# Optimization experiments

Measured on AMD Instinct MI355X. Metric: run time of the kernel, lower is better.

The kernel has to match this reference:

```python
import jax, jax.numpy as jnp
import numpy as np

T, N, E = 64, 10000, 160000
NIN, NHID, NOUT = 64, 128, 64

def _xavier(key, shape):
    # xavier_normal_ for Linear/GCNConv lin weights of shape [out, in]
    std = jnp.sqrt(2.0 / (shape[0] + shape[1])).astype(jnp.float32)
    return std * jax.random.normal(key, shape, dtype=jnp.float32)

def setup_inputs() -> dict:
    key = jax.random.key(0)
    ks = jax.random.split(key, 12)
    x = jax.random.normal(ks[0], (T, N, NIN), dtype=jnp.float32)
    src = jax.random.randint(ks[1], (E,), 0, N)
    dst = jax.random.randint(ks[2], (E,), 0, N)
    edge_index = jnp.stack([src, dst])  # [2, E], PyG convention src->dst
    m_in = dst   # receiver index per edge (one-hot row of incidence matrix)
    m_out = src  # sender index per edge
    b = 0.1 * jnp.ones((NHID,), jnp.float32)
    return {
        "x": x, "edge_index": edge_index, "m_in": m_in, "m_out": m_out,
        "Wi": _xavier(ks[3], (NHID, NIN + NHID)), "bi": b,
        "Wf": _xavier(ks[4], (NHID, NIN + NHID)), "bf": b,
        "Wo": _xavier(ks[5], (NHID, NIN + NHID)), "bo": b,
        "Wg": _xavier(ks[6], (NHID, NIN + NHID)), "bg": b,
        "W1": _xavier(ks[7], (NHID, 2 * NHID)), "b1": b,
        "Wc": _xavier(ks[8], (NOUT, NHID)), "bc": 0.1 * jnp.ones((NOUT,), jnp.float32),
    }

def reference(x, edge_index, m_in, m_out, Wi, bi, Wf, bf, Wo, bo, Wg, bg, W1, b1, Wc, bc):
    n = x.shape[1]
    src, dst = edge_index[0], edge_index[1]
    loop = jnp.arange(n)
    s = jnp.concatenate([src, loop])  # self-loops appended (GCNConv default)
    d = jnp.concatenate([dst, loop])
    deg = jax.ops.segment_sum(jnp.ones_like(d, x.dtype), d, num_segments=n)
    dinv = jnp.where(deg > 0, deg, 1.0) ** -0.5  # deg>=1 with self-loops
    norm = (dinv[s] * dinv[d])[:, None]

    def gcn(z, W, b):
        zw = z @ W.T                    # [n, out]
        return jax.ops.segment_sum(zw[s] * norm, d, num_segments=n) + b

    def step(carry, xt):
        h, c = carry
        comb = jnp.concatenate([xt, h], axis=-1)  # [n, n_in+n_hid]
        i = jax.nn.sigmoid(gcn(comb, Wi, bi))
        f = jax.nn.sigmoid(gcn(comb, Wf, bf))
        o = jax.nn.sigmoid(gcn(comb, Wo, bo))
        g = jnp.tanh(gcn(comb, Wg, bg))
        c = f * c + i * g
        h = o * jnp.tanh(c)
        return (h, c), None

    h0 = jnp.zeros((n, NHID), x.dtype)
    (h, _), _ = jax.lax.scan(step, (h0, h0), x)

    # node2edge: concat receiver and sender hidden states  [E, 2*n_hid]
    e = jnp.concatenate([h[m_in], h[m_out]], axis=-1)
    e = jax.nn.relu(e @ W1.T + b1)  # dropout p=0.0 -> identity
    # edge2node: scatter-sum edge features to receiver nodes
    nodes = jax.ops.segment_sum(e, m_in, num_segments=n)
    return gcn(nodes, Wc, bc)
```

## Files before the change

### kernel.cpp

```cpp
#include <hip/hip_runtime.h>
#include <math.h>

#define NIN 64
#define NHID 128
#define NOUT 64

typedef __bf16 bf16x8 __attribute__((ext_vector_type(8)));
typedef float  floatx4 __attribute__((ext_vector_type(4)));

__device__ __forceinline__ float sigmoidf(float x){ return 1.0f/(1.0f+expf(-x)); }
__device__ __forceinline__ float b2f_lo(unsigned p){ unsigned b = p<<16; return __uint_as_float(b); }
__device__ __forceinline__ float b2f_hi(unsigned p){ unsigned b = p & 0xffff0000u; return __uint_as_float(b); }
__device__ __forceinline__ unsigned f2pk(float lo, float hi){
  __bf16 a=(__bf16)lo, b=(__bf16)hi;
  unsigned short ua, ub;
  __builtin_memcpy(&ua,&a,2); __builtin_memcpy(&ub,&b,2);
  return (unsigned)ua | ((unsigned)ub<<16);
}

__global__ void k_deg_init(int* __restrict__ deg, int n){
  int v = blockIdx.x*256 + threadIdx.x;
  if(v<n) deg[v] = 1;
}
__global__ void k_deg_count(const int* __restrict__ dst, int E, int* __restrict__ deg){
  int e = blockIdx.x*256 + threadIdx.x;
  if(e<E) atomicAdd(&deg[dst[e]], 1);
}
__global__ void k_dinv(const int* __restrict__ deg, float* __restrict__ dinv, int n){
  int v = blockIdx.x*256 + threadIdx.x;
  if(v<n) dinv[v] = rsqrtf((float)deg[v]);
}
__global__ __launch_bounds__(1024) void k_scan(const int* __restrict__ deg,
    int* __restrict__ row_ptr, int* __restrict__ fill, int n){
  __shared__ int lds[1024];
  __shared__ int s_carry;
  if(threadIdx.x==0) s_carry=0;
  __syncthreads();
  int nchunk=(n+1023)/1024;
  for(int ch=0; ch<nchunk; ++ch){
    int v = ch*1024 + threadIdx.x;
    int val = (v<n)? (deg[v]-1) : 0;
    lds[threadIdx.x]=val;
    __syncthreads();
    for(int off=1; off<1024; off<<=1){
      int t=(threadIdx.x>=off)? lds[threadIdx.x-off] : 0;
      __syncthreads();
      lds[threadIdx.x]+=t;
      __syncthreads();
    }
    int incl=lds[threadIdx.x];
    int carry=s_carry;
    if(v<n){ row_ptr[v]=carry+incl-val; fill[v]=carry+incl-val; }
    __syncthreads();
    if(threadIdx.x==1023) s_carry=carry+lds[1023];
    __syncthreads();
  }
  if(threadIdx.x==0) row_ptr[n]=s_carry;
}
__global__ void k_fill(const int* __restrict__ src, const int* __restrict__ dst, int E,
                       int* __restrict__ fill, int* __restrict__ ecol){
  int e = blockIdx.x*256 + threadIdx.x;
  if(e<E){
    int d = dst[e];
    int pos = atomicAdd(&fill[d], 1);
    ecol[pos] = src[e];
  }
}

__global__ void k_prep_wb(const float* __restrict__ Wi, const float* __restrict__ Wf,
                          const float* __restrict__ Wo, const float* __restrict__ Wg,
                          __bf16* __restrict__ Wb){
  int idx = blockIdx.x*256 + threadIdx.x;
  if(idx >= 32*6*64*8) return;
  int jj = idx & 7;
  int L  = (idx >> 3) & 63;
  int t  = idx >> 9;
  int kt = t - (t/6)*6, CT = t/6;
  int colj = CT*16 + (L & 15);
  int k    = kt*32 + ((L >> 4) << 3) + jj;
  int gate = colj >> 7, jg = colj & 127;
  const float* W = (gate==0)? Wi : (gate==1)? Wf : (gate==2)? Wo : Wg;
  Wb[idx] = (__bf16)W[jg*192 + k];
}
__global__ void k_prep_w1(const float* __restrict__ W1, float* __restrict__ W1t){
  int idx = blockIdx.x*256 + threadIdx.x;
  if(idx >= 128*256) return;
  int k = idx >> 8, j = idx & 255;
  W1t[idx] = (j<128)? W1[j*256+k] : W1[(j-128)*256+128+k];
}
__global__ void k_prep_wc(const float* __restrict__ Wc, float* __restrict__ Wct){
  int idx = blockIdx.x*256 + threadIdx.x;
  if(idx >= 128*64) return;
  int k = idx/64, j = idx%64;
  Wct[idx] = Wc[j*128+k];
}

__global__ void k_init(unsigned* __restrict__ hpA, unsigned* __restrict__ hpB,
                       float* __restrict__ cbuf, __bf16* __restrict__ xs,
                       int NP, int T){
  int i = blockIdx.x*256 + threadIdx.x;
  if(i < (NP+1)*64){ hpA[i]=0u; hpB[i]=0u; }
  if(i < NP*128) cbuf[i]=0.f;
  if(i < T*64){ int t=i>>6, f=i&63; xs[((size_t)t*(NP+1) + NP)*64 + f] = (__bf16)0.f; }
}

__global__ void k_xscale(const float* __restrict__ x, const float* __restrict__ dinv,
                         __bf16* __restrict__ xs, int n, int NP){
  int i = blockIdx.x*256 + threadIdx.x;
  if(i >= n*8) return;
  int t = blockIdx.y;
  float dv = dinv[i>>3];
  const float4* xp = (const float4*)(x + (size_t)t*(size_t)n*64) + (size_t)i*2;
  float4 a = xp[0], b = xp[1];
  bf16x8 o;
  o[0]=(__bf16)(a.x*dv); o[1]=(__bf16)(a.y*dv); o[2]=(__bf16)(a.z*dv); o[3]=(__bf16)(a.w*dv);
  o[4]=(__bf16)(b.x*dv); o[5]=(__bf16)(b.y*dv); o[6]=(__bf16)(b.z*dv); o[7]=(__bf16)(b.w*dv);
  *(bf16x8*)(xs + ((size_t)t*(NP+1))*64 + (size_t)i*8) = o;
}

__global__ __launch_bounds__(256,4) void k_step(
    const __bf16* __restrict__ xst,
    const unsigned* __restrict__ hp_prev,
    unsigned* __restrict__ hp_cur,
    float* __restrict__ cbuf,
    float* __restrict__ hbuf,
    const int* __restrict__ row_ptr, const int* __restrict__ ecol,
    const float* __restrict__ dinv, const __bf16* __restrict__ Wb,
    const float* __restrict__ bi, const float* __restrict__ bf_,
    const float* __restrict__ bo, const float* __restrict__ bg,
    int n, int NP, int last)
{
  __shared__ __align__(16) __bf16 s_a[6*544];
  __shared__ int   s_col[1024];
  __shared__ int   s_deg[16];
  __shared__ int   s_beg[16];
  __shared__ float s_dv[16];
  const int tid=threadIdx.x, wv=tid>>6, l=tid&63;
  const int l15=l&15, quad=l>>4;
  const int v0=blockIdx.x*16;

  if(tid<16){
    int v=v0+tid;
    int beg=(v<n)? row_ptr[v]:0, end=(v<n)? row_ptr[v+1]:0;
    s_beg[tid]=beg; s_deg[tid]=end-beg;
    s_dv[tid]=(v<n)? dinv[v]:0.f;
  }
  __syncthreads();
  for(int idx=tid; idx<1024; idx+=256){
    int m=idx>>6, kk=idx&63;
    s_col[idx]=(kk<s_deg[m])? ecol[s_beg[m]+kk] : NP;
  }
  __syncthreads();

  float ax[4], alo[4], ahi[4];
  int K;
  {
    int d0=s_deg[4*wv+0]; d0=d0>64?64:d0;
    int d1=s_deg[4*wv+1]; d1=d1>64?64:d1;
    int d2=s_deg[4*wv+2]; d2=d2>64?64:d2;
    int d3=s_deg[4*wv+3]; d3=d3>64?64:d3;
    int m01=d0>d1?d0:d1, m23=d2>d3?d2:d3;
    K=m01>m23?m01:m23;
  }
  #pragma unroll
  for(int i=0;i<4;++i){
    int v=v0+4*wv+i;
    ax[i]=(float)xst[(size_t)v*64+l];
    unsigned p=hp_prev[(size_t)v*64+l];
    alo[i]=b2f_lo(p); ahi[i]=b2f_hi(p);
  }
  const int* cr=&s_col[(4*wv)*64];
  #pragma unroll 2
  for(int kk=0;kk<K;++kk){
    #pragma unroll
    for(int i=0;i<4;++i){
      int u=cr[i*64+kk];
      float xv=(float)xst[(size_t)u*64+l];
      unsigned p=hp_prev[(size_t)u*64+l];
      ax[i]+=xv; alo[i]+=b2f_lo(p); ahi[i]+=b2f_hi(p);
    }
  }
  #pragma unroll
  for(int i=0;i<4;++i){
    int m=4*wv+i, d=s_deg[m];
    if(d>64){
      for(int e2=s_beg[m]+64;e2<s_beg[m]+d;++e2){
        int u=ecol[e2];
        ax[i]+=(float)xst[(size_t)u*64+l];
        unsigned p=hp_prev[(size_t)u*64+l];
        alo[i]+=b2f_lo(p); ahi[i]+=b2f_hi(p);
      }
    }
  }
  {
    int kt0=l>>5, q0=(l>>3)&3, j0=l&7;
    int L2=2*l, kt1=2+(L2>>5), q1=(L2>>3)&3, j1=L2&7;
    #pragma unroll
    for(int i=0;i<4;++i){
      int m=4*wv+i; float dv=s_dv[m];
      s_a[kt0*544+q0*136+m*8+j0]=(__bf16)(dv*ax[i]);
      *(__shared__ unsigned*)&s_a[kt1*544+q1*136+m*8+j1]=f2pk(dv*alo[i],dv*ahi[i]);
    }
  }
  __syncthreads();

  bf16x8 af[6];
  #pragma unroll
  for(int kt=0;kt<6;++kt)
    af[kt]=*(__shared__ bf16x8*)&s_a[kt*544+quad*136+l15*8];

  #pragma unroll
  for(int h2=0;h2<2;++h2){
    const int ct=2*wv+h2;
    const int jg=16*ct+l15;
    floatx4 acc[4];
    #pragma unroll
    for(int g=0;g<4;++g){
      const float* bsel = (g==0)? bi : (g==1)? bf_ : (g==2)? bo : bg;
      float b=bsel[jg];
      floatx4 a={b,b,b,b};
      const __bf16* bp=Wb + (size_t)((8*g+ct)*6)*512 + (size_t)l*8;
      #pragma unroll
      for(int kt=0;kt<6;++kt)
        a=__builtin_amdgcn_mfma_f32_16x16x32_bf16(af[kt],*(const bf16x8*)(bp+kt*512),a,0,0,0);
      acc[g]=a;
    }
    #pragma unroll
    for(int r=0;r<4;++r){
      int m=quad*4+r, v=v0+m;
      float I=sigmoidf(acc[0][r]);
      float F=sigmoidf(acc[1][r]);
      float O=sigmoidf(acc[2][r]);
      float G=tanhf  (acc[3][r]);
      size_t coff=(size_t)v*128+jg;
      float cn=F*cbuf[coff]+I*G;
      cbuf[coff]=cn;
      float hn=O*tanhf(cn);
      float hs=s_dv[m]*hn;
      float hs2=__shfl_xor(hs,1,64);
      if((l15&1)==0)
        hp_cur[(size_t)v*64+(jg>>1)]=f2pk(hs,hs2);
      if(last) hbuf[coff]=hn;
    }
  }
}

__global__ __launch_bounds__(256) void k_head1(const float* __restrict__ h,
    const float* __restrict__ W1t, float* __restrict__ Hio, int n){
  __shared__ float s_h[16][NHID];
  int v0 = blockIdx.x*16;
  for(int i=threadIdx.x; i<16*NHID; i+=256){
    int m = i/NHID, k = i - m*NHID;
    int v = v0 + m;
    s_h[m][k] = (v<n)? h[(size_t)v*NHID + k] : 0.0f;
  }
  __syncthreads();
  int j = threadIdx.x;
  float acc[16];
  #pragma unroll
  for(int m=0;m<16;++m) acc[m]=0.f;
  for(int k=0;k<NHID;++k){
    float w = W1t[k*256 + j];
    #pragma unroll
    for(int m=0;m<16;++m) acc[m] = fmaf(w, s_h[m][k], acc[m]);
  }
  for(int m=0;m<16;++m){
    int v = v0 + m;
    if(v >= n) break;
    Hio[(size_t)v*256 + j] = acc[m];
  }
}
__global__ __launch_bounds__(256) void k_e2n(const float* __restrict__ Hio,
    const int* __restrict__ row_ptr, const int* __restrict__ col,
    const float* __restrict__ b1, float* __restrict__ nodes, int n){
  int wv = threadIdx.x >> 6, lane = threadIdx.x & 63;
  int v = blockIdx.x*4 + wv;
  if(v >= n) return;
  float base0 = Hio[(size_t)v*256 + lane]      + b1[lane];
  float base1 = Hio[(size_t)v*256 + 64 + lane] + b1[64+lane];
  float a0=0.f, a1=0.f;
  int beg=row_ptr[v], end=row_ptr[v+1];
  int e=beg;
  for(; e+1<end; e+=2){
    int u0 = col[e], u1 = col[e+1];
    float p0 = Hio[(size_t)u0*256 + 128 + lane];
    float q0 = Hio[(size_t)u0*256 + 192 + lane];
    float p1 = Hio[(size_t)u1*256 + 128 + lane];
    float q1 = Hio[(size_t)u1*256 + 192 + lane];
    a0 += fmaxf(base0 + p0, 0.0f) + fmaxf(base0 + p1, 0.0f);
    a1 += fmaxf(base1 + q0, 0.0f) + fmaxf(base1 + q1, 0.0f);
  }
  if(e<end){
    int u = col[e];
    a0 += fmaxf(base0 + Hio[(size_t)u*256 + 128 + lane], 0.0f);
    a1 += fmaxf(base1 + Hio[(size_t)u*256 + 192 + lane], 0.0f);
  }
  nodes[(size_t)v*NHID + lane]      = a0;
  nodes[(size_t)v*NHID + 64 + lane] = a1;
}
__global__ __launch_bounds__(64) void k_head2(const float* __restrict__ nodes,
    const float* __restrict__ Wct, float* __restrict__ tmp, int n){
  __shared__ float s_n[16][NHID];
  int v0 = blockIdx.x*16;
  for(int i=threadIdx.x; i<16*NHID; i+=64){
    int m = i/NHID, k = i - m*NHID;
    int v = v0 + m;
    s_n[m][k] = (v<n)? nodes[(size_t)v*NHID + k] : 0.0f;
  }
  __syncthreads();
  int j = threadIdx.x;
  float acc[16];
  #pragma unroll
  for(int m=0;m<16;++m) acc[m]=0.f;
  for(int k=0;k<NHID;++k){
    float w = Wct[k*64 + j];
    #pragma unroll
    for(int m=0;m<16;++m) acc[m] = fmaf(w, s_n[m][k], acc[m]);
  }
  for(int m=0;m<16;++m){
    int v = v0 + m;
    if(v >= n) break;
    tmp[(size_t)v*64 + j] = acc[m];
  }
}
__global__ __launch_bounds__(256) void k_final(const float* __restrict__ tmp,
    const int* __restrict__ row_ptr, const int* __restrict__ col,
    const float* __restrict__ dinv, const float* __restrict__ bc,
    float* __restrict__ out, int n){
  int wv = threadIdx.x >> 6, lane = threadIdx.x & 63;
  int v = blockIdx.x*4 + wv;
  if(v >= n) return;
  float dv = dinv[v];
  float acc = dv*dv*tmp[(size_t)v*64 + lane];
  int beg=row_ptr[v], end=row_ptr[v+1];
  int e=beg;
  for(; e+1<end; e+=2){
    int u0 = col[e], u1 = col[e+1];
    float d0 = dinv[u0], d1 = dinv[u1];
    float t0 = tmp[(size_t)u0*64 + lane];
    float t1 = tmp[(size_t)u1*64 + lane];
    acc = fmaf(dv*d0, t0, acc);
    acc = fmaf(dv*d1, t1, acc);
  }
  if(e<end){
    int u = col[e];
    acc = fmaf(dv*dinv[u], tmp[(size_t)u*64 + lane], acc);
  }
  out[(size_t)v*64 + lane] = acc + bc[lane];
}

extern "C" void kernel_launch(void* const* d_in, const int* in_sizes, int n_in,
                              void* d_out, int out_size, void* d_ws, size_t ws_size,
                              hipStream_t stream) {
  (void)n_in; (void)ws_size;
  const float* x  = (const float*)d_in[0];
  const int*   ei = (const int*)d_in[1];
  const float* Wi = (const float*)d_in[4];  const float* bi  = (const float*)d_in[5];
  const float* Wf = (const float*)d_in[6];  const float* bf_ = (const float*)d_in[7];
  const float* Wo = (const float*)d_in[8];  const float* bo  = (const float*)d_in[9];
  const float* Wg = (const float*)d_in[10]; const float* bg  = (const float*)d_in[11];
  const float* W1 = (const float*)d_in[12]; const float* b1  = (const float*)d_in[13];
  const float* Wc = (const float*)d_in[14]; const float* bc  = (const float*)d_in[15];
  float* out = (float*)d_out;

  const int E = in_sizes[2];
  const int n = out_size / NOUT;
  const int T = in_sizes[0] / (n * NIN);
  const int ntiles = (n + 15)/16;
  const int NP = ntiles*16;
  const int* srcl = ei;
  const int* dstl = ei + E;

  char* p = (char*)d_ws;
  auto alloc = [&](size_t bytes){ char* r = p; p += ((bytes + 255)/256)*256; return r; };
  int*      deg     = (int*)     alloc((size_t)n*4);
  float*    dinv    = (float*)   alloc((size_t)n*4);
  int*      row_ptr = (int*)     alloc((size_t)(n+1)*4);
  int*      fill    = (int*)     alloc((size_t)n*4);
  int*      ecol    = (int*)     alloc((size_t)E*4);
  __bf16*   Wb      = (__bf16*)  alloc((size_t)32*6*64*8*2);
  float*    W1t     = (float*)   alloc((size_t)128*256*4);
  float*    Wct     = (float*)   alloc((size_t)128*64*4);
  __bf16*   xs      = (__bf16*)  alloc((size_t)T*(NP+1)*64*2);
  unsigned* hpA     = (unsigned*)alloc((size_t)(NP+1)*64*4);
  unsigned* hpB     = (unsigned*)alloc((size_t)(NP+1)*64*4);
  float*    cbuf    = (float*)   alloc((size_t)NP*128*4);
  float*    hbuf    = (float*)   alloc((size_t)NP*128*4);
  float*    Hio     = (float*)   alloc((size_t)NP*256*4);
  float*    nodes   = (float*)   alloc((size_t)n*NHID*4);
  float*    tmp     = (float*)   alloc((size_t)NP*64*4);

  int gn = (n+255)/256;
  int gE = (E+255)/256;

  k_deg_init <<<gn, 256, 0, stream>>>(deg, n);
  k_deg_count<<<gE, 256, 0, stream>>>(dstl, E, deg);
  k_dinv     <<<gn, 256, 0, stream>>>(deg, dinv, n);
  k_scan     <<<1, 1024, 0, stream>>>(deg, row_ptr, fill, n);
  k_fill     <<<gE, 256, 0, stream>>>(srcl, dstl, E, fill, ecol);

  k_prep_wb<<<(32*6*64*8+255)/256, 256, 0, stream>>>(Wi, Wf, Wo, Wg, Wb);
  k_prep_w1<<<(128*256+255)/256, 256, 0, stream>>>(W1, W1t);
  k_prep_wc<<<(128*64+255)/256, 256, 0, stream>>>(Wc, Wct);

  k_init<<<((NP*128)+255)/256, 256, 0, stream>>>(hpA, hpB, cbuf, xs, NP, T);
  k_xscale<<<dim3((n*8+255)/256, T), 256, 0, stream>>>(x, dinv, xs, n, NP);

  for(int t=0; t<T; ++t){
    const __bf16* xst = xs + (size_t)t*(size_t)(NP+1)*64;
    const unsigned* hp = (t & 1)? hpB : hpA;
    unsigned*       hc = (t & 1)? hpA : hpB;
    k_step<<<ntiles, 256, 0, stream>>>(xst, hp, hc, cbuf, hbuf, row_ptr, ecol, dinv,
                                       Wb, bi, bf_, bo, bg, n, NP, (t==T-1)?1:0);
  }

  k_head1<<<ntiles, 256, 0, stream>>>(hbuf, W1t, Hio, n);
  k_e2n  <<<(n+3)/4, 256, 0, stream>>>(Hio, row_ptr, ecol, b1, nodes, n);
  k_head2<<<(n+15)/16, 64, 0, stream>>>(nodes, Wct, tmp, n);
  k_final<<<(n+3)/4, 256, 0, stream>>>(tmp, row_ptr, ecol, dinv, bc, out, n);
}
```

Baseline: 1.789 ms.

## Precompute x-part neighbor aggregation for all timesteps outside the recurrent loop

The GCN aggregation of the input features x does not depend on the hidden state, so it is moved out of the 64 sequential step kernels into one batched k_xgather kernel. That kernel writes pre-normalized bf16 A-tiles in MFMA layout for every timestep. The step kernel now gathers only neighbor hidden states and loads the x tiles directly into registers. It also runs with 512 threads, one output column tile per wave, which spreads the gate computation across more waves per block. The cost is extra memory for the precomputed tiles and an fp32 gather over x done before the loop.

```diff
diff --git a/kernel.cpp b/kernel.cpp
--- a/kernel.cpp
+++ b/kernel.cpp
@@ -96,30 +96,84 @@
 }
 
 __global__ void k_init(unsigned* __restrict__ hpA, unsigned* __restrict__ hpB,
-                       float* __restrict__ cbuf, __bf16* __restrict__ xs,
-                       int NP, int T){
+                       float* __restrict__ cbuf, int NP){
   int i = blockIdx.x*256 + threadIdx.x;
   if(i < (NP+1)*64){ hpA[i]=0u; hpB[i]=0u; }
   if(i < NP*128) cbuf[i]=0.f;
-  if(i < T*64){ int t=i>>6, f=i&63; xs[((size_t)t*(NP+1) + NP)*64 + f] = (__bf16)0.f; }
-}
-
-__global__ void k_xscale(const float* __restrict__ x, const float* __restrict__ dinv,
-                         __bf16* __restrict__ xs, int n, int NP){
-  int i = blockIdx.x*256 + threadIdx.x;
-  if(i >= n*8) return;
-  int t = blockIdx.y;
-  float dv = dinv[i>>3];
-  const float4* xp = (const float4*)(x + (size_t)t*(size_t)n*64) + (size_t)i*2;
-  float4 a = xp[0], b = xp[1];
-  bf16x8 o;
-  o[0]=(__bf16)(a.x*dv); o[1]=(__bf16)(a.y*dv); o[2]=(__bf16)(a.z*dv); o[3]=(__bf16)(a.w*dv);
-  o[4]=(__bf16)(b.x*dv); o[5]=(__bf16)(b.y*dv); o[6]=(__bf16)(b.z*dv); o[7]=(__bf16)(b.w*dv);
-  *(bf16x8*)(xs + ((size_t)t*(NP+1))*64 + (size_t)i*8) = o;
-}
-
-__global__ __launch_bounds__(256,4) void k_step(
-    const __bf16* __restrict__ xst,
+}
+
+__global__ __launch_bounds__(256) void k_xgather(
+    const float* __restrict__ x, const int* __restrict__ row_ptr,
+    const int* __restrict__ ecol, const float* __restrict__ dinv,
+    __bf16* __restrict__ gaxF, int n, int ntiles)
+{
+  __shared__ int   s_col[1024];
+  __shared__ int   s_deg[16];
+  __shared__ int   s_beg[16];
+  __shared__ float s_dv[16];
+  const int tid=threadIdx.x, wv=tid>>6, l=tid&63;
+  const int v0=blockIdx.x*16;
+  const int t=blockIdx.y;
+  const float* xt = x + (size_t)t*(size_t)n*64;
+
+  if(tid<16){
+    int v=v0+tid;
+    int beg=(v<n)? row_ptr[v]:0, end=(v<n)? row_ptr[v+1]:0;
+    s_beg[tid]=beg; s_deg[tid]=end-beg;
+    s_dv[tid]=(v<n)? dinv[v]:0.f;
+  }
+  __syncthreads();
+  for(int idx=tid; idx<1024; idx+=256){
+    int m=idx>>6, kk=idx&63;
+    s_col[idx]=(kk<s_deg[m])? ecol[s_beg[m]+kk] : n;
+  }
+  __syncthreads();
+
+  float ax[4];
+  int K;
+  {
+    int d0=s_deg[4*wv+0]; d0=d0>64?64:d0;
+    int d1=s_deg[4*wv+1]; d1=d1>64?64:d1;
+    int d2=s_deg[4*wv+2]; d2=d2>64?64:d2;
+    int d3=s_deg[4*wv+3]; d3=d3>64?64:d3;
+    int m01=d0>d1?d0:d1, m23=d2>d3?d2:d3;
+    K=m01>m23?m01:m23;
+  }
+  #pragma unroll
+  for(int i=0;i<4;++i){
+    int v=v0+4*wv+i;
+    ax[i]=(v<n)? s_dv[4*wv+i]*xt[(size_t)v*64+l] : 0.f;
+  }
+  const int* cr=&s_col[(4*wv)*64];
+  #pragma unroll 2
+  for(int kk=0;kk<K;++kk){
+    #pragma unroll
+    for(int i=0;i<4;++i){
+      int u=cr[i*64+kk];
+      if(u<n) ax[i] += dinv[u]*xt[(size_t)u*64+l];
+    }
+  }
+  #pragma unroll
+  for(int i=0;i<4;++i){
+    int m=4*wv+i, d=s_deg[m];
+    if(d>64){
+      for(int e2=s_beg[m]+64;e2<s_beg[m]+d;++e2){
+        int u=ecol[e2];
+        ax[i]+=dinv[u]*xt[(size_t)u*64+l];
+      }
+    }
+  }
+  size_t base=((size_t)t*ntiles + blockIdx.x)*1024;
+  int kt=l>>5, q=(l>>3)&3, j=l&7;
+  #pragma unroll
+  for(int i=0;i<4;++i){
+    int m=4*wv+i;
+    gaxF[base + (size_t)kt*512 + q*128 + m*8 + j] = (__bf16)(s_dv[m]*ax[i]);
+  }
+}
+
+__global__ __launch_bounds__(512,5) void k_step(
+    const __bf16* __restrict__ gax,
     const unsigned* __restrict__ hp_prev,
     unsigned* __restrict__ hp_cur,
     float* __restrict__ cbuf,
@@ -130,7 +184,7 @@
     const float* __restrict__ bo, const float* __restrict__ bg,
     int n, int NP, int last)
 {
-  __shared__ __align__(16) __bf16 s_a[6*544];
+  __shared__ __align__(16) __bf16 s_a[4*544];
   __shared__ int   s_col[1024];
   __shared__ int   s_deg[16];
   __shared__ int   s_beg[16];
@@ -146,102 +200,96 @@
     s_dv[tid]=(v<n)? dinv[v]:0.f;
   }
   __syncthreads();
-  for(int idx=tid; idx<1024; idx+=256){
+  for(int idx=tid; idx<1024; idx+=512){
     int m=idx>>6, kk=idx&63;
     s_col[idx]=(kk<s_deg[m])? ecol[s_beg[m]+kk] : NP;
   }
   __syncthreads();
 
-  float ax[4], alo[4], ahi[4];
+  float alo[2], ahi[2];
   int K;
   {
-    int d0=s_deg[4*wv+0]; d0=d0>64?64:d0;
-    int d1=s_deg[4*wv+1]; d1=d1>64?64:d1;
-    int d2=s_deg[4*wv+2]; d2=d2>64?64:d2;
-    int d3=s_deg[4*wv+3]; d3=d3>64?64:d3;
-    int m01=d0>d1?d0:d1, m23=d2>d3?d2:d3;
-    K=m01>m23?m01:m23;
-  }
-  #pragma unroll
-  for(int i=0;i<4;++i){
-    int v=v0+4*wv+i;
-    ax[i]=(float)xst[(size_t)v*64+l];
+    int d0=s_deg[2*wv], d1=s_deg[2*wv+1];
+    d0=d0>64?64:d0; d1=d1>64?64:d1;
+    K=d0>d1?d0:d1;
+  }
+  #pragma unroll
+  for(int i=0;i<2;++i){
+    int v=v0+2*wv+i;
     unsigned p=hp_prev[(size_t)v*64+l];
     alo[i]=b2f_lo(p); ahi[i]=b2f_hi(p);
   }
-  const int* cr=&s_col[(4*wv)*64];
+  const int* cr=&s_col[(2*wv)*64];
   #pragma unroll 2
   for(int kk=0;kk<K;++kk){
-    #pragma unroll
-    for(int i=0;i<4;++i){
-      int u=cr[i*64+kk];
-      float xv=(float)xst[(size_t)u*64+l];
-      unsigned p=hp_prev[(size_t)u*64+l];
-      ax[i]+=xv; alo[i]+=b2f_lo(p); ahi[i]+=b2f_hi(p);
-    }
-  }
-  #pragma unroll
-  for(int i=0;i<4;++i){
-    int m=4*wv+i, d=s_deg[m];
+    int u0=cr[kk], u1=cr[64+kk];
+    unsigned p0=hp_prev[(size_t)u0*64+l];
+    unsigned p1=hp_prev[(size_t)u1*64+l];
+    alo[0]+=b2f_lo(p0); ahi[0]+=b2f_hi(p0);
+    alo[1]+=b2f_lo(p1); ahi[1]+=b2f_hi(p1);
+  }
+  #pragma unroll
+  for(int i=0;i<2;++i){
+    int m=2*wv+i, d=s_deg[m];
     if(d>64){
       for(int e2=s_beg[m]+64;e2<s_beg[m]+d;++e2){
         int u=ecol[e2];
-        ax[i]+=(float)xst[(size_t)u*64+l];
         unsigned p=hp_prev[(size_t)u*64+l];
         alo[i]+=b2f_lo(p); ahi[i]+=b2f_hi(p);
       }
     }
   }
   {
-    int kt0=l>>5, q0=(l>>3)&3, j0=l&7;
-    int L2=2*l, kt1=2+(L2>>5), q1=(L2>>3)&3, j1=L2&7;
+    int L2=2*l, slab=(L2>>5), q1=(L2>>3)&3, j1=L2&7;
     #pragma unroll
-    for(int i=0;i<4;++i){
-      int m=4*wv+i; float dv=s_dv[m];
-      s_a[kt0*544+q0*136+m*8+j0]=(__bf16)(dv*ax[i]);
-      *(__shared__ unsigned*)&s_a[kt1*544+q1*136+m*8+j1]=f2pk(dv*alo[i],dv*ahi[i]);
+    for(int i=0;i<2;++i){
+      int m=2*wv+i; float dv=s_dv[m];
+      *(__shared__ unsigned*)&s_a[slab*544+q1*136+m*8+j1]=f2pk(dv*alo[i],dv*ahi[i]);
     }
   }
   __syncthreads();
 
   bf16x8 af[6];
-  #pragma unroll
-  for(int kt=0;kt<6;++kt)
-    af[kt]=*(__shared__ bf16x8*)&s_a[kt*544+quad*136+l15*8];
-
-  #pragma unroll
-  for(int h2=0;h2<2;++h2){
-    const int ct=2*wv+h2;
-    const int jg=16*ct+l15;
-    floatx4 acc[4];
+  {
+    const __bf16* gx = gax + (size_t)blockIdx.x*1024;
+    af[0]=*(const bf16x8*)&gx[quad*128+l15*8];
+    af[1]=*(const bf16x8*)&gx[512+quad*128+l15*8];
+  }
+  #pragma unroll
+  for(int kt=2;kt<6;++kt)
+    af[kt]=*(__shared__ bf16x8*)&s_a[(kt-2)*544+quad*136+l15*8];
+  const int jg=16*wv+l15;
+  floatx4 acc[4];
+  {
     #pragma unroll
     for(int g=0;g<4;++g){
       const float* bsel = (g==0)? bi : (g==1)? bf_ : (g==2)? bo : bg;
       float b=bsel[jg];
       floatx4 a={b,b,b,b};
-      const __bf16* bp=Wb + (size_t)((8*g+ct)*6)*512 + (size_t)l*8;
+      const __bf16* bp=Wb + (size_t)((8*g+wv)*6)*512 + (size_t)l*8;
       #pragma unroll
       for(int kt=0;kt<6;++kt)
         a=__builtin_amdgcn_mfma_f32_16x16x32_bf16(af[kt],*(const bf16x8*)(bp+kt*512),a,0,0,0);
       acc[g]=a;
     }
-    #pragma unroll
-    for(int r=0;r<4;++r){
-      int m=quad*4+r, v=v0+m;
-      float I=sigmoidf(acc[0][r]);
-      float F=sigmoidf(acc[1][r]);
-      float O=sigmoidf(acc[2][r]);
-      float G=tanhf  (acc[3][r]);
-      size_t coff=(size_t)v*128+jg;
-      float cn=F*cbuf[coff]+I*G;
-      cbuf[coff]=cn;
-      float hn=O*tanhf(cn);
-      float hs=s_dv[m]*hn;
-      float hs2=__shfl_xor(hs,1,64);
-      if((l15&1)==0)
-        hp_cur[(size_t)v*64+(jg>>1)]=f2pk(hs,hs2);
-      if(last) hbuf[coff]=hn;
-    }
+  }
+
+  #pragma unroll
+  for(int r=0;r<4;++r){
+    int m=quad*4+r, v=v0+m;
+    float I=sigmoidf(acc[0][r]);
+    float F=sigmoidf(acc[1][r]);
+    float O=sigmoidf(acc[2][r]);
+    float G=tanhf  (acc[3][r]);
+    size_t coff=(size_t)v*128+jg;
+    float cn=F*cbuf[coff]+I*G;
+    cbuf[coff]=cn;
+    float hn=O*tanhf(cn);
+    float hs=s_dv[m]*hn;
+    float hs2=__shfl_xor(hs,1,64);
+    if((l15&1)==0)
+      hp_cur[(size_t)v*64+(jg>>1)]=f2pk(hs,hs2);
+    if(last) hbuf[coff]=hn;
   }
 }
 
@@ -381,7 +429,7 @@
   __bf16*   Wb      = (__bf16*)  alloc((size_t)32*6*64*8*2);
   float*    W1t     = (float*)   alloc((size_t)128*256*4);
   float*    Wct     = (float*)   alloc((size_t)128*64*4);
-  __bf16*   xs      = (__bf16*)  alloc((size_t)T*(NP+1)*64*2);
+  __bf16*   gaxF    = (__bf16*)  alloc((size_t)T*ntiles*1024*2);
   unsigned* hpA     = (unsigned*)alloc((size_t)(NP+1)*64*4);
   unsigned* hpB     = (unsigned*)alloc((size_t)(NP+1)*64*4);
   float*    cbuf    = (float*)   alloc((size_t)NP*128*4);
@@ -403,14 +451,14 @@
   k_prep_w1<<<(128*256+255)/256, 256, 0, stream>>>(W1, W1t);
   k_prep_wc<<<(128*64+255)/256, 256, 0, stream>>>(Wc, Wct);
 
-  k_init<<<((NP*128)+255)/256, 256, 0, stream>>>(hpA, hpB, cbuf, xs, NP, T);
-  k_xscale<<<dim3((n*8+255)/256, T), 256, 0, stream>>>(x, dinv, xs, n, NP);
+  k_init<<<((NP*128)+255)/256, 256, 0, stream>>>(hpA, hpB, cbuf, NP);
+  k_xgather<<<dim3(ntiles, T), 256, 0, stream>>>(x, row_ptr, ecol, dinv, gaxF, n, ntiles);
 
   for(int t=0; t<T; ++t){
-    const __bf16* xst = xs + (size_t)t*(size_t)(NP+1)*64;
+    const __bf16* gax_t = gaxF + (size_t)t*(size_t)ntiles*1024;
     const unsigned* hp = (t & 1)? hpB : hpA;
     unsigned*       hc = (t & 1)? hpA : hpB;
-    k_step<<<ntiles, 256, 0, stream>>>(xst, hp, hc, cbuf, hbuf, row_ptr, ecol, dinv,
+    k_step<<<ntiles, 512, 0, stream>>>(gax_t, hp, hc, cbuf, hbuf, row_ptr, ecol, dinv,
                                        Wb, bi, bf_, bo, bg, n, NP, (t==T-1)?1:0);
   }
 
```

Result: slower. 2.071 ms (+15.7%).

## Interleave x and h into one gather buffer and use 512-thread step blocks

Applied to the files above, without the earlier changes.

The per-step gather now reads a single interleaved uint2 buffer that packs the next step's scaled x feature with the packed h pair, so each neighbour fetch is one 8-byte load instead of two separate loads from the x and h arrays. Each step kernel writes the next step's x into this combined buffer alongside the new h, and the t=0 buffer is seeded in k_xscale. Blocks grow to 512 threads (8 waves), with each wave gathering 2 nodes and computing one column tile, which raises parallelism per tile of 16 nodes. The cost is extra write traffic (copying x into the combined buffer every step), a larger buffer footprint, and possible register or occupancy pressure from the new launch bounds.

```diff
diff --git a/kernel.cpp b/kernel.cpp
--- a/kernel.cpp
+++ b/kernel.cpp
@@ -95,17 +95,16 @@
   Wct[idx] = Wc[j*128+k];
 }
 
-__global__ void k_init(unsigned* __restrict__ hpA, unsigned* __restrict__ hpB,
-                       float* __restrict__ cbuf, __bf16* __restrict__ xs,
-                       int NP, int T){
+__global__ void k_init(uint2* __restrict__ combA, uint2* __restrict__ combB,
+                       float* __restrict__ cbuf, int NP){
   int i = blockIdx.x*256 + threadIdx.x;
-  if(i < (NP+1)*64){ hpA[i]=0u; hpB[i]=0u; }
+  if(i < (NP+1)*64){ combA[i]=make_uint2(0u,0u); combB[i]=make_uint2(0u,0u); }
   if(i < NP*128) cbuf[i]=0.f;
-  if(i < T*64){ int t=i>>6, f=i&63; xs[((size_t)t*(NP+1) + NP)*64 + f] = (__bf16)0.f; }
 }
 
 __global__ void k_xscale(const float* __restrict__ x, const float* __restrict__ dinv,
-                         __bf16* __restrict__ xs, int n, int NP){
+                         __bf16* __restrict__ xs, uint2* __restrict__ combA,
+                         int n, int NP){
   int i = blockIdx.x*256 + threadIdx.x;
   if(i >= n*8) return;
   int t = blockIdx.y;
@@ -116,12 +115,21 @@
   o[0]=(__bf16)(a.x*dv); o[1]=(__bf16)(a.y*dv); o[2]=(__bf16)(a.z*dv); o[3]=(__bf16)(a.w*dv);
   o[4]=(__bf16)(b.x*dv); o[5]=(__bf16)(b.y*dv); o[6]=(__bf16)(b.z*dv); o[7]=(__bf16)(b.w*dv);
   *(bf16x8*)(xs + ((size_t)t*(NP+1))*64 + (size_t)i*8) = o;
-}
-
-__global__ __launch_bounds__(256,4) void k_step(
-    const __bf16* __restrict__ xst,
-    const unsigned* __restrict__ hp_prev,
-    unsigned* __restrict__ hp_cur,
+  if(t==0){
+    int v = i>>3, f0 = (i&7)*8;
+    #pragma unroll
+    for(int j=0;j<8;++j){
+      __bf16 bj = o[j];
+      unsigned short us; __builtin_memcpy(&us,&bj,2);
+      combA[(size_t)v*64 + f0 + j] = make_uint2((unsigned)us, 0u);
+    }
+  }
+}
+
+__global__ __launch_bounds__(512,5) void k_step(
+    const uint2* __restrict__ comb_prev,
+    uint2* __restrict__ comb_cur,
+    const __bf16* __restrict__ xs1,
     float* __restrict__ cbuf,
     float* __restrict__ hbuf,
     const int* __restrict__ row_ptr, const int* __restrict__ ecol,
@@ -146,49 +154,42 @@
     s_dv[tid]=(v<n)? dinv[v]:0.f;
   }
   __syncthreads();
-  for(int idx=tid; idx<1024; idx+=256){
+  for(int idx=tid; idx<1024; idx+=512){
     int m=idx>>6, kk=idx&63;
     s_col[idx]=(kk<s_deg[m])? ecol[s_beg[m]+kk] : NP;
   }
   __syncthreads();
 
-  float ax[4], alo[4], ahi[4];
+  float ax[2], alo[2], ahi[2];
   int K;
   {
-    int d0=s_deg[4*wv+0]; d0=d0>64?64:d0;
-    int d1=s_deg[4*wv+1]; d1=d1>64?64:d1;
-    int d2=s_deg[4*wv+2]; d2=d2>64?64:d2;
-    int d3=s_deg[4*wv+3]; d3=d3>64?64:d3;
-    int m01=d0>d1?d0:d1, m23=d2>d3?d2:d3;
-    K=m01>m23?m01:m23;
-  }
-  #pragma unroll
-  for(int i=0;i<4;++i){
-    int v=v0+4*wv+i;
-    ax[i]=(float)xst[(size_t)v*64+l];
-    unsigned p=hp_prev[(size_t)v*64+l];
-    alo[i]=b2f_lo(p); ahi[i]=b2f_hi(p);
-  }
-  const int* cr=&s_col[(4*wv)*64];
+    int d0=s_deg[2*wv], d1=s_deg[2*wv+1];
+    d0=d0>64?64:d0; d1=d1>64?64:d1;
+    K=d0>d1?d0:d1;
+  }
+  #pragma unroll
+  for(int i=0;i<2;++i){
+    int v=v0+2*wv+i;
+    uint2 w=comb_prev[(size_t)v*64+l];
+    ax[i]=b2f_lo(w.x); alo[i]=b2f_lo(w.y); ahi[i]=b2f_hi(w.y);
+  }
+  const int* cr=&s_col[(2*wv)*64];
   #pragma unroll 2
   for(int kk=0;kk<K;++kk){
-    #pragma unroll
-    for(int i=0;i<4;++i){
-      int u=cr[i*64+kk];
-      float xv=(float)xst[(size_t)u*64+l];
-      unsigned p=hp_prev[(size_t)u*64+l];
-      ax[i]+=xv; alo[i]+=b2f_lo(p); ahi[i]+=b2f_hi(p);
-    }
-  }
-  #pragma unroll
-  for(int i=0;i<4;++i){
-    int m=4*wv+i, d=s_deg[m];
+    int u0=cr[kk], u1=cr[64+kk];
+    uint2 w0=comb_prev[(size_t)u0*64+l];
+    uint2 w1=comb_prev[(size_t)u1*64+l];
+    ax[0]+=b2f_lo(w0.x); alo[0]+=b2f_lo(w0.y); ahi[0]+=b2f_hi(w0.y);
+    ax[1]+=b2f_lo(w1.x); alo[1]+=b2f_lo(w1.y); ahi[1]+=b2f_hi(w1.y);
+  }
+  #pragma unroll
+  for(int i=0;i<2;++i){
+    int m=2*wv+i, d=s_deg[m];
     if(d>64){
       for(int e2=s_beg[m]+64;e2<s_beg[m]+d;++e2){
         int u=ecol[e2];
-        ax[i]+=(float)xst[(size_t)u*64+l];
-        unsigned p=hp_prev[(size_t)u*64+l];
-        alo[i]+=b2f_lo(p); ahi[i]+=b2f_hi(p);
+        uint2 w=comb_prev[(size_t)u*64+l];
+        ax[i]+=b2f_lo(w.x); alo[i]+=b2f_lo(w.y); ahi[i]+=b2f_hi(w.y);
       }
     }
   }
@@ -196,10 +197,10 @@
     int kt0=l>>5, q0=(l>>3)&3, j0=l&7;
     int L2=2*l, kt1=2+(L2>>5), q1=(L2>>3)&3, j1=L2&7;
     #pragma unroll
-    for(int i=0;i<4;++i){
-      int m=4*wv+i; float dv=s_dv[m];
+    for(int i=0;i<2;++i){
+      int m=2*wv+i; float dv=s_dv[m];
       s_a[kt0*544+q0*136+m*8+j0]=(__bf16)(dv*ax[i]);
-      *(__shared__ unsigned*)&s_a[kt1*544+q1*136+m*8+j1]=f2pk(dv*alo[i],dv*ahi[i]);
+      *(unsigned*)&s_a[kt1*544+q1*136+m*8+j1]=f2pk(dv*alo[i],dv*ahi[i]);
     }
   }
   __syncthreads();
@@ -207,41 +208,43 @@
   bf16x8 af[6];
   #pragma unroll
   for(int kt=0;kt<6;++kt)
-    af[kt]=*(__shared__ bf16x8*)&s_a[kt*544+quad*136+l15*8];
-
-  #pragma unroll
-  for(int h2=0;h2<2;++h2){
-    const int ct=2*wv+h2;
-    const int jg=16*ct+l15;
-    floatx4 acc[4];
+    af[kt]=*(bf16x8*)&s_a[kt*544+quad*136+l15*8];
+  const int jg=16*wv+l15;
+  floatx4 acc[4];
+  {
     #pragma unroll
     for(int g=0;g<4;++g){
       const float* bsel = (g==0)? bi : (g==1)? bf_ : (g==2)? bo : bg;
       float b=bsel[jg];
       floatx4 a={b,b,b,b};
-      const __bf16* bp=Wb + (size_t)((8*g+ct)*6)*512 + (size_t)l*8;
+      const __bf16* bp=Wb + (size_t)((8*g+wv)*6)*512 + (size_t)l*8;
       #pragma unroll
       for(int kt=0;kt<6;++kt)
         a=__builtin_amdgcn_mfma_f32_16x16x32_bf16(af[kt],*(const bf16x8*)(bp+kt*512),a,0,0,0);
       acc[g]=a;
     }
-    #pragma unroll
-    for(int r=0;r<4;++r){
-      int m=quad*4+r, v=v0+m;
-      float I=sigmoidf(acc[0][r]);
-      float F=sigmoidf(acc[1][r]);
-      float O=sigmoidf(acc[2][r]);
-      float G=tanhf  (acc[3][r]);
-      size_t coff=(size_t)v*128+jg;
-      float cn=F*cbuf[coff]+I*G;
-      cbuf[coff]=cn;
-      float hn=O*tanhf(cn);
-      float hs=s_dv[m]*hn;
-      float hs2=__shfl_xor(hs,1,64);
-      if((l15&1)==0)
-        hp_cur[(size_t)v*64+(jg>>1)]=f2pk(hs,hs2);
-      if(last) hbuf[coff]=hn;
-    }
+  }
+
+  #pragma unroll
+  for(int r=0;r<4;++r){
+    int m=quad*4+r, v=v0+m;
+    float I=sigmoidf(acc[0][r]);
+    float F=sigmoidf(acc[1][r]);
+    float O=sigmoidf(acc[2][r]);
+    float G=tanhf  (acc[3][r]);
+    size_t coff=(size_t)v*128+jg;
+    float cn=F*cbuf[coff]+I*G;
+    cbuf[coff]=cn;
+    float hn=O*tanhf(cn);
+    float hs=s_dv[m]*hn;
+    float hs2=__shfl_xor(hs,1,64);
+    if((l15&1)==0){
+      int w = jg>>1;
+      unsigned short us;
+      __builtin_memcpy(&us, &xs1[(size_t)v*64 + w], 2);
+      comb_cur[(size_t)v*64 + w] = make_uint2((unsigned)us, f2pk(hs,hs2));
+    }
+    if(last) hbuf[coff]=hn;
   }
 }
 
@@ -382,8 +385,8 @@
   float*    W1t     = (float*)   alloc((size_t)128*256*4);
   float*    Wct     = (float*)   alloc((size_t)128*64*4);
   __bf16*   xs      = (__bf16*)  alloc((size_t)T*(NP+1)*64*2);
-  unsigned* hpA     = (unsigned*)alloc((size_t)(NP+1)*64*4);
-  unsigned* hpB     = (unsigned*)alloc((size_t)(NP+1)*64*4);
+  uint2*    combA   = (uint2*)   alloc((size_t)(NP+1)*64*8);
+  uint2*    combB   = (uint2*)   alloc((size_t)(NP+1)*64*8);
   float*    cbuf    = (float*)   alloc((size_t)NP*128*4);
   float*    hbuf    = (float*)   alloc((size_t)NP*128*4);
   float*    Hio     = (float*)   alloc((size_t)NP*256*4);
@@ -403,14 +406,15 @@
   k_prep_w1<<<(128*256+255)/256, 256, 0, stream>>>(W1, W1t);
   k_prep_wc<<<(128*64+255)/256, 256, 0, stream>>>(Wc, Wct);
 
-  k_init<<<((NP*128)+255)/256, 256, 0, stream>>>(hpA, hpB, cbuf, xs, NP, T);
-  k_xscale<<<dim3((n*8+255)/256, T), 256, 0, stream>>>(x, dinv, xs, n, NP);
+  k_init<<<((NP*128)+255)/256, 256, 0, stream>>>(combA, combB, cbuf, NP);
+  k_xscale<<<dim3((n*8+255)/256, T), 256, 0, stream>>>(x, dinv, xs, combA, n, NP);
 
   for(int t=0; t<T; ++t){
-    const __bf16* xst = xs + (size_t)t*(size_t)(NP+1)*64;
-    const unsigned* hp = (t & 1)? hpB : hpA;
-    unsigned*       hc = (t & 1)? hpA : hpB;
-    k_step<<<ntiles, 256, 0, stream>>>(xst, hp, hc, cbuf, hbuf, row_ptr, ecol, dinv,
+    int t1 = (t+1 < T)? (t+1) : (T-1);
+    const __bf16* xs1 = xs + (size_t)t1*(size_t)(NP+1)*64;
+    const uint2* cp = (t & 1)? combB : combA;
+    uint2*       cc = (t & 1)? combA : combB;
+    k_step<<<ntiles, 512, 0, stream>>>(cp, cc, xs1, cbuf, hbuf, row_ptr, ecol, dinv,
                                        Wb, bi, bf_, bo, bg, n, NP, (t==T-1)?1:0);
   }
 
```

New measurement: 1.831 ms. +2.3%, slower.

## Use 512-thread blocks processing two node tiles each in LSTM step kernel

Applied to the files above, without the earlier changes.

The per-timestep GCN-LSTM kernel now launches half as many blocks of 512 threads. Each block handles two 16-node tiles in sequence, with each wave gathering neighbours for 2 nodes instead of 4 and computing one MFMA column tile instead of two. The aim is more memory-level parallelism in the gather and less per-wave serial work and register pressure. The cost is extra block-wide barriers between the two tiles and a different occupancy target (launch bounds 512,5).

```diff
diff --git a/kernel.cpp b/kernel.cpp
--- a/kernel.cpp
+++ b/kernel.cpp
@@ -118,7 +118,7 @@
   *(bf16x8*)(xs + ((size_t)t*(NP+1))*64 + (size_t)i*8) = o;
 }
 
-__global__ __launch_bounds__(256,4) void k_step(
+__global__ __launch_bounds__(512,5) void k_step(
     const __bf16* __restrict__ xst,
     const unsigned* __restrict__ hp_prev,
     unsigned* __restrict__ hp_cur,
@@ -128,120 +128,129 @@
     const float* __restrict__ dinv, const __bf16* __restrict__ Wb,
     const float* __restrict__ bi, const float* __restrict__ bf_,
     const float* __restrict__ bo, const float* __restrict__ bg,
-    int n, int NP, int last)
+    int n, int NP, int last, int ntiles)
 {
   __shared__ __align__(16) __bf16 s_a[6*544];
-  __shared__ int   s_col[1024];
-  __shared__ int   s_deg[16];
-  __shared__ int   s_beg[16];
-  __shared__ float s_dv[16];
+  __shared__ int   s_col[2][1024];
+  __shared__ int   s_deg[2][16];
+  __shared__ int   s_beg[2][16];
+  __shared__ float s_dv[2][16];
   const int tid=threadIdx.x, wv=tid>>6, l=tid&63;
   const int l15=l&15, quad=l>>4;
-  const int v0=blockIdx.x*16;
-
-  if(tid<16){
-    int v=v0+tid;
-    int beg=(v<n)? row_ptr[v]:0, end=(v<n)? row_ptr[v+1]:0;
-    s_beg[tid]=beg; s_deg[tid]=end-beg;
-    s_dv[tid]=(v<n)? dinv[v]:0.f;
+  const int G = gridDim.x;
+
+  if(tid<32){
+    int p=tid>>4, q=tid&15;
+    int tile=blockIdx.x+p*G;
+    int v=tile*16+q;
+    bool val=(tile<ntiles)&&(v<n);
+    int beg=val? row_ptr[v]:0, end=val? row_ptr[v+1]:0;
+    s_beg[p][q]=beg; s_deg[p][q]=end-beg;
+    s_dv[p][q]=val? dinv[v]:0.f;
   }
   __syncthreads();
-  for(int idx=tid; idx<1024; idx+=256){
-    int m=idx>>6, kk=idx&63;
-    s_col[idx]=(kk<s_deg[m])? ecol[s_beg[m]+kk] : NP;
+  for(int idx=tid; idx<2048; idx+=512){
+    int p=idx>>10, m=(idx>>6)&15, kk=idx&63;
+    s_col[p][idx&1023]=(kk<s_deg[p][m])? ecol[s_beg[p][m]+kk] : NP;
   }
   __syncthreads();
 
-  float ax[4], alo[4], ahi[4];
-  int K;
-  {
-    int d0=s_deg[4*wv+0]; d0=d0>64?64:d0;
-    int d1=s_deg[4*wv+1]; d1=d1>64?64:d1;
-    int d2=s_deg[4*wv+2]; d2=d2>64?64:d2;
-    int d3=s_deg[4*wv+3]; d3=d3>64?64:d3;
-    int m01=d0>d1?d0:d1, m23=d2>d3?d2:d3;
-    K=m01>m23?m01:m23;
-  }
+  const int jg=16*wv+l15;
+
   #pragma unroll
-  for(int i=0;i<4;++i){
-    int v=v0+4*wv+i;
-    ax[i]=(float)xst[(size_t)v*64+l];
-    unsigned p=hp_prev[(size_t)v*64+l];
-    alo[i]=b2f_lo(p); ahi[i]=b2f_hi(p);
-  }
-  const int* cr=&s_col[(4*wv)*64];
-  #pragma unroll 2
-  for(int kk=0;kk<K;++kk){
-    #pragma unroll
-    for(int i=0;i<4;++i){
-      int u=cr[i*64+kk];
-      float xv=(float)xst[(size_t)u*64+l];
-      unsigned p=hp_prev[(size_t)u*64+l];
-      ax[i]+=xv; alo[i]+=b2f_lo(p); ahi[i]+=b2f_hi(p);
+  for(int p=0;p<2;++p){
+    const int tile = blockIdx.x+p*G;
+    const int v0 = tile*16;
+    const bool tval = (tile<ntiles);
+
+    if(tval){
+      float ax[2], alo[2], ahi[2];
+      int d0=s_deg[p][2*wv], d1=s_deg[p][2*wv+1];
+      bool ovf=(d0>64)||(d1>64);
+      d0=d0>64?64:d0; d1=d1>64?64:d1;
+      const int K=d0>d1?d0:d1;
+      #pragma unroll
+      for(int i=0;i<2;++i){
+        int v=v0+2*wv+i;
+        ax[i]=(float)xst[(size_t)v*64+l];
+        unsigned pw=hp_prev[(size_t)v*64+l];
+        alo[i]=b2f_lo(pw); ahi[i]=b2f_hi(pw);
+      }
+      const int* cr=&s_col[p][(2*wv)*64];
+      #pragma unroll 2
+      for(int kk=0;kk<K;++kk){
+        int u0=cr[kk], u1=cr[64+kk];
+        float    x0=(float)xst[(size_t)u0*64+l];
+        unsigned p0=hp_prev[(size_t)u0*64+l];
+        float    x1=(float)xst[(size_t)u1*64+l];
+        unsigned p1=hp_prev[(size_t)u1*64+l];
+        ax[0]+=x0; alo[0]+=b2f_lo(p0); ahi[0]+=b2f_hi(p0);
+        ax[1]+=x1; alo[1]+=b2f_lo(p1); ahi[1]+=b2f_hi(p1);
+      }
+      if(ovf){
+        #pragma unroll
+        for(int i=0;i<2;++i){
+          int m=2*wv+i, d=s_deg[p][m];
+          if(d>64){
+            for(int e2=s_beg[p][m]+64;e2<s_beg[p][m]+d;++e2){
+              int u=ecol[e2];
+              ax[i]+=(float)xst[(size_t)u*64+l];
+              unsigned pw=hp_prev[(size_t)u*64+l];
+              alo[i]+=b2f_lo(pw); ahi[i]+=b2f_hi(pw);
+            }
+          }
+        }
+      }
+      {
+        int kt0=l>>5, q0=(l>>3)&3, j0=l&7;
+        int L2=2*l, kt1=2+(L2>>5), q1=(L2>>3)&3, j1=L2&7;
+        #pragma unroll
+        for(int i=0;i<2;++i){
+          int m=2*wv+i; float dv=s_dv[p][m];
+          s_a[kt0*544+q0*136+m*8+j0]=(__bf16)(dv*ax[i]);
+          *(unsigned*)&s_a[kt1*544+q1*136+m*8+j1]=f2pk(dv*alo[i],dv*ahi[i]);
+        }
+      }
     }
-  }
-  #pragma unroll
-  for(int i=0;i<4;++i){
-    int m=4*wv+i, d=s_deg[m];
-    if(d>64){
-      for(int e2=s_beg[m]+64;e2<s_beg[m]+d;++e2){
-        int u=ecol[e2];
-        ax[i]+=(float)xst[(size_t)u*64+l];
-        unsigned p=hp_prev[(size_t)u*64+l];
-        alo[i]+=b2f_lo(p); ahi[i]+=b2f_hi(p);
-      }
-    }
-  }
-  {
-    int kt0=l>>5, q0=(l>>3)&3, j0=l&7;
-    int L2=2*l, kt1=2+(L2>>5), q1=(L2>>3)&3, j1=L2&7;
-    #pragma unroll
-    for(int i=0;i<4;++i){
-      int m=4*wv+i; float dv=s_dv[m];
-      s_a[kt0*544+q0*136+m*8+j0]=(__bf16)(dv*ax[i]);
-      *(__shared__ unsigned*)&s_a[kt1*544+q1*136+m*8+j1]=f2pk(dv*alo[i],dv*ahi[i]);
-    }
-  }
-  __syncthreads();
-
-  bf16x8 af[6];
-  #pragma unroll
-  for(int kt=0;kt<6;++kt)
-    af[kt]=*(__shared__ bf16x8*)&s_a[kt*544+quad*136+l15*8];
-
-  #pragma unroll
-  for(int h2=0;h2<2;++h2){
-    const int ct=2*wv+h2;
-    const int jg=16*ct+l15;
-    floatx4 acc[4];
-    #pragma unroll
-    for(int g=0;g<4;++g){
-      const float* bsel = (g==0)? bi : (g==1)? bf_ : (g==2)? bo : bg;
-      float b=bsel[jg];
-      floatx4 a={b,b,b,b};
-      const __bf16* bp=Wb + (size_t)((8*g+ct)*6)*512 + (size_t)l*8;
+    __syncthreads();
+
+    if(tval){
+      bf16x8 af[6];
       #pragma unroll
       for(int kt=0;kt<6;++kt)
-        a=__builtin_amdgcn_mfma_f32_16x16x32_bf16(af[kt],*(const bf16x8*)(bp+kt*512),a,0,0,0);
-      acc[g]=a;
+        af[kt]=*(bf16x8*)&s_a[kt*544+quad*136+l15*8];
+      floatx4 acc[4];
+      #pragma unroll
+      for(int g=0;g<4;++g){
+        const float* bsel = (g==0)? bi : (g==1)? bf_ : (g==2)? bo : bg;
+        float b=bsel[jg];
+        floatx4 a={b,b,b,b};
+        const __bf16* bp=Wb + (size_t)((8*g+wv)*6)*512 + (size_t)l*8;
+        #pragma unroll
+        for(int kt=0;kt<6;++kt)
+          a=__builtin_amdgcn_mfma_f32_16x16x32_bf16(af[kt],*(const bf16x8*)(bp+kt*512),a,0,0,0);
+        acc[g]=a;
+      }
+
+      #pragma unroll
+      for(int r=0;r<4;++r){
+        int m=quad*4+r, v=v0+m;
+        float I=sigmoidf(acc[0][r]);
+        float F=sigmoidf(acc[1][r]);
+        float O=sigmoidf(acc[2][r]);
+        float Gg=tanhf (acc[3][r]);
+        size_t coff=(size_t)v*128+jg;
+        float cn=F*cbuf[coff]+I*Gg;
+        cbuf[coff]=cn;
+        float hn=O*tanhf(cn);
+        float hs=s_dv[p][m]*hn;
+        float hs2=__shfl_xor(hs,1,64);
+        if((l15&1)==0)
+          hp_cur[(size_t)v*64+(jg>>1)]=f2pk(hs,hs2);
+        if(last) hbuf[coff]=hn;
+      }
     }
-    #pragma unroll
-    for(int r=0;r<4;++r){
-      int m=quad*4+r, v=v0+m;
-      float I=sigmoidf(acc[0][r]);
-      float F=sigmoidf(acc[1][r]);
-      float O=sigmoidf(acc[2][r]);
-      float G=tanhf  (acc[3][r]);
-      size_t coff=(size_t)v*128+jg;
-      float cn=F*cbuf[coff]+I*G;
-      cbuf[coff]=cn;
-      float hn=O*tanhf(cn);
-      float hs=s_dv[m]*hn;
-      float hs2=__shfl_xor(hs,1,64);
-      if((l15&1)==0)
-        hp_cur[(size_t)v*64+(jg>>1)]=f2pk(hs,hs2);
-      if(last) hbuf[coff]=hn;
-    }
+    __syncthreads();
   }
 }
 
@@ -406,12 +415,15 @@
   k_init<<<((NP*128)+255)/256, 256, 0, stream>>>(hpA, hpB, cbuf, xs, NP, T);
   k_xscale<<<dim3((n*8+255)/256, T), 256, 0, stream>>>(x, dinv, xs, n, NP);
 
-  for(int t=0; t<T; ++t){
-    const __bf16* xst = xs + (size_t)t*(size_t)(NP+1)*64;
-    const unsigned* hp = (t & 1)? hpB : hpA;
-    unsigned*       hc = (t & 1)? hpA : hpB;
-    k_step<<<ntiles, 256, 0, stream>>>(xst, hp, hc, cbuf, hbuf, row_ptr, ecol, dinv,
-                                       Wb, bi, bf_, bo, bg, n, NP, (t==T-1)?1:0);
+  {
+    const int G = (ntiles+1)/2;
+    for(int t=0; t<T; ++t){
+      const __bf16* xst = xs + (size_t)t*(size_t)(NP+1)*64;
+      const unsigned* hp = (t & 1)? hpB : hpA;
+      unsigned*       hc = (t & 1)? hpA : hpB;
+      k_step<<<G, 512, 0, stream>>>(xst, hp, hc, cbuf, hbuf, row_ptr, ecol, dinv,
+                                    Wb, bi, bf_, bo, bg, n, NP, (t==T-1)?1:0, ntiles);
+    }
   }
 
   k_head1<<<ntiles, 256, 0, stream>>>(hbuf, W1t, Hio, n);
```

Result: slower. 2.202 ms (+23.0%).
